# Kernel optimization log

Hardware: AMD Instinct MI355X
Metric: run time of the kernel (lower is better)

## Reference

```python
import jax, jax.numpy as jnp
import numpy as np

B, S, K = 8, 128, 12          # batch, seq len, nPredicts
DAR, DENC = 256, 256          # AR dim, encoder dim
NNEG = 128                    # negativeSamplingExt
W = S - K                     # windowSize


def setup_inputs() -> dict:
    key = jax.random.key(0)
    k1, k2, k3, k4, k5 = jax.random.split(key, 5)
    cFeature = jax.random.normal(k1, (B, S, DAR), dtype=jnp.float32)
    encodedData = jax.random.normal(k2, (B, S, DENC), dtype=jnp.float32)
    # stacked bias-free Linear weights, one per prediction step k
    Wpred = jax.random.normal(k3, (K, DENC, DAR), dtype=jnp.float32) / jnp.sqrt(DAR)
    n_idx = NNEG * W * B
    batchIdx = jax.random.randint(k4, (n_idx,), 0, B, dtype=jnp.int32)
    seqIdx = jax.random.randint(k5, (n_idx,), 1, S, dtype=jnp.int32)  # low=1 as in torch
    return {"cFeature": cFeature, "encodedData": encodedData, "Wpred": Wpred,
            "batchIdx": batchIdx, "seqIdx": seqIdx}


def reference(cFeature, encodedData, Wpred, batchIdx, seqIdx):
    c = cFeature[:, :W]                                   # (B, W, DAR)
    flat = encodedData.reshape(-1, DENC)                  # (B*S, DENC)

    # sampleClean: baseIdx arange(W) broadcast over (B, NNEG, W) then flattened
    base = jnp.tile(jnp.arange(W, dtype=jnp.int32), B * NNEG)
    seq = (seqIdx + base) % S
    ext = seq + batchIdx * S
    negExt = flat[ext].reshape(B, NNEG, W, DENC)          # irregular gather, ~121 MB

    # per-k linear prediction: locC[k] = c @ Wpred[k].T
    locC = jnp.einsum('bwd,ked->kbwe', c, Wpred)          # (K, B, W, DENC)

    # positives: encodedData[:, k:k+W] for k = 1..K
    pos = jnp.stack([encodedData[:, k:k + W] for k in range(1, K + 1)])  # (K, B, W, DENC)

    # (locC * candidates).mean(dim=feature) == dot / DENC
    posScore = jnp.einsum('kbwe,kbwe->kbw', locC, pos) / DENC           # (K, B, W)
    negScore = jnp.einsum('kbwe,bnwe->kbnw', locC, negExt) / DENC       # (K, B, N, W)

    logits = jnp.concatenate([posScore[:, :, None, :], negScore], axis=2)  # (K, B, 1+N, W)
    logits = jnp.transpose(logits, (0, 1, 3, 2)).reshape(K, B * W, 1 + NNEG)

    # cross entropy with label 0 (positive at class index 0)
    lse = jax.nn.logsumexp(logits, axis=-1)               # (K, B*W)
    losses = jnp.mean(lse - logits[..., 0], axis=-1)      # (K,)
    accs = jnp.mean((jnp.argmax(logits, axis=-1) == 0).astype(jnp.float32), axis=-1)
    return losses[None, :], accs[None, :]                  # (1, K), (1, K)
```

## Files before the change

kernel.cpp:

```cpp
#include <hip/hip_runtime.h>
#include <math.h>

#define B_    8
#define S_    128
#define K_    12
#define DAR_  256
#define DENC_ 256
#define NNEG_ 128
#define W_    116
#define BW_   928

typedef __attribute__((ext_vector_type(8))) short short8;
typedef __attribute__((ext_vector_type(4))) float floatx4;

static __device__ __forceinline__ unsigned short f2bf(float f) {
    union { float f; unsigned int u; } v; v.f = f;
    return (unsigned short)((v.u + 0x7FFFu + ((v.u >> 16) & 1u)) >> 16);
}

__global__ __launch_bounds__(256) void cast_all(
    const float* __restrict__ enc, const float* __restrict__ cf,
    const float* __restrict__ wp,
    unsigned short* __restrict__ ench, unsigned short* __restrict__ cfh,
    unsigned short* __restrict__ wph)
{
    const int g = blockIdx.x * 256 + threadIdx.x;
    const float* src; unsigned short* dst; int off;
    if (g < 32768)      { src = enc; dst = ench; off = g * 8; }
    else if (g < 65536) { src = cf;  dst = cfh;  off = (g - 32768) * 8; }
    else                { src = wp;  dst = wph;  off = (g - 65536) * 8; }
    float4 v0 = *(const float4*)(src + off);
    float4 v1 = *(const float4*)(src + off + 4);
    uint4 o;
    o.x = f2bf(v0.x) | ((unsigned)f2bf(v0.y) << 16);
    o.y = f2bf(v0.z) | ((unsigned)f2bf(v0.w) << 16);
    o.z = f2bf(v1.x) | ((unsigned)f2bf(v1.y) << 16);
    o.w = f2bf(v1.z) | ((unsigned)f2bf(v1.w) << 16);
    *(uint4*)(dst + off) = o;
}

__global__ __launch_bounds__(256) void stage1_mfma(
    const unsigned short* __restrict__ cfh,
    const unsigned short* __restrict__ wph,
    unsigned short* __restrict__ locCh)
{
    __shared__ unsigned short Bh[64 * 256];

    const int tid = threadIdx.x;
    const int mt = blockIdx.x;
    const int nt = blockIdx.y;
    const int k  = blockIdx.z;

    const int lane = tid & 63, wv = tid >> 6;
    const int l15 = lane & 15, quad = lane >> 4;

    const int am = mt * 64 + wv * 16 + l15;
    const bool avalid = (am < BW_);
    short8 a[8];
    if (avalid) {
        const int b = am / W_, w = am - b * W_;
        const unsigned short* arow = cfh + (size_t)(b * S_ + w) * 256;
#pragma unroll
        for (int kt = 0; kt < 8; ++kt)
            a[kt] = *(const short8*)(arow + kt * 32 + quad * 8);
    } else {
#pragma unroll
        for (int kt = 0; kt < 8; ++kt) a[kt] = short8{0,0,0,0,0,0,0,0};
    }

#pragma unroll
    for (int i = 0; i < 8; ++i) {
        const int flat = i * 256 + tid;
        const int row = flat >> 5, ch = flat & 31;
        const int e = nt * 64 + row;
        uint4 bv = *(const uint4*)(wph + ((size_t)(k * 256 + e) * 256 + ch * 8));
        *(uint4*)&Bh[(row * 32 + (ch ^ (row & 7))) * 8] = bv;
    }
    __syncthreads();

    floatx4 acc[4];
#pragma unroll
    for (int n4 = 0; n4 < 4; ++n4) {
        floatx4 c = {0.f, 0.f, 0.f, 0.f};
        const int bn = n4 * 16 + l15;
#pragma unroll
        for (int kt = 0; kt < 8; ++kt) {
            const int ch = kt * 4 + quad;
            short8 bfrag = *(const short8*)&Bh[(bn * 32 + (ch ^ (bn & 7))) * 8];
            c = __builtin_amdgcn_mfma_f32_16x16x32_bf16(a[kt], bfrag, c, 0, 0, 0);
        }
        acc[n4] = c;
    }

#pragma unroll
    for (int n4 = 0; n4 < 4; ++n4) {
        const int e = nt * 64 + n4 * 16 + l15;
#pragma unroll
        for (int r = 0; r < 4; ++r) {
            const int bwo = mt * 64 + wv * 16 + quad * 4 + r;
            if (bwo < BW_)
                locCh[((size_t)k * BW_ + bwo) * 256 + e] = f2bf(acc[r < 0 ? 0 : n4][r]);
        }
    }
}

__global__ __launch_bounds__(256) void stage2_mfma(
    const unsigned short* __restrict__ ench,
    const unsigned short* __restrict__ locCh,
    const int* __restrict__ batchIdx,
    const int* __restrict__ seqIdx,
    float* __restrict__ part)
{
    __shared__ int   idxL[144];
    __shared__ float sc[K_ * 132];

    const int tid = threadIdx.x;
    const int bw = blockIdx.x;
    const int b = bw / W_, w = bw - b * W_;

    const int lane = tid & 63, wv = tid >> 6;
    const int l15 = lane & 15, quad = lane >> 4;

    const int m = (l15 < K_) ? l15 : (K_ - 1);
    const unsigned short* arow = locCh + ((size_t)m * BW_ + bw) * 256;
    short8 a[8];
#pragma unroll
    for (int kt = 0; kt < 8; ++kt)
        a[kt] = *(const short8*)(arow + kt * 32 + quad * 8);

    if (tid < NNEG_) {
        const int ii = (b * NNEG_ + tid) * W_ + w;
        const int bi = batchIdx[ii];
        int si = seqIdx[ii] + w;
        if (si >= S_) si -= S_;
        idxL[tid] = bi * S_ + si;
    } else if (tid < 140) {
        idxL[tid] = b * S_ + w + 1 + (tid - 128);
    }
    __syncthreads();

    floatx4 accT[3];
#pragma unroll
    for (int u = 0; u < 3; ++u) {
        const int t = wv + u * 4;
        floatx4 c = {0.f, 0.f, 0.f, 0.f};
        if (t < 9) {
            const int n = t * 16 + l15;
            const int nn = (n < 140) ? n : 128;
            const unsigned short* brow = ench + (size_t)idxL[nn] * 256;
#pragma unroll
            for (int kt = 0; kt < 8; ++kt) {
                short8 bfrag = *(const short8*)(brow + kt * 32 + quad * 8);
                c = __builtin_amdgcn_mfma_f32_16x16x32_bf16(a[kt], bfrag, c, 0, 0, 0);
            }
        }
        accT[u] = c;
    }

    const float inv = 1.0f / 256.0f;
#pragma unroll
    for (int u = 0; u < 3; ++u) {
        const int t = wv + u * 4;
        if (t < 9) {
#pragma unroll
            for (int r = 0; r < 4; ++r) {
                const int mm = quad * 4 + r;
                if (mm < K_) {
                    const float val = accT[u][r] * inv;
                    if (t < 8)           sc[mm * 132 + t * 16 + l15] = val;
                    else if (l15 == mm)  sc[mm * 132 + 128] = val;
                }
            }
        }
    }
    __syncthreads();

    for (int k = wv; k < K_; k += 4) {
        const float x0  = sc[k * 132 + lane];
        const float x1  = sc[k * 132 + 64 + lane];
        const float pos = sc[k * 132 + 128];
        float mn = fmaxf(x0, x1);
#pragma unroll
        for (int o = 1; o < 64; o <<= 1) mn = fmaxf(mn, __shfl_xor(mn, o, 64));
        const float m2 = fmaxf(mn, pos);
        float s = __expf(x0 - m2) + __expf(x1 - m2);
#pragma unroll
        for (int o = 1; o < 64; o <<= 1) s += __shfl_xor(s, o, 64);
        if (lane == 0) {
            const float lse = m2 + __logf(s + __expf(pos - m2));
            part[k * BW_ + bw]        = lse - pos;
            part[(K_ + k) * BW_ + bw] = (pos >= mn) ? 1.0f : 0.0f;
        }
    }
}

__global__ __launch_bounds__(256) void stage3_reduce(
    const float* __restrict__ part, float* __restrict__ out)
{
    __shared__ float wsum[4];
    const int o = blockIdx.x, tid = threadIdx.x;
    float s = 0.f;
    for (int i = tid; i < BW_; i += 256) s += part[o * BW_ + i];
#pragma unroll
    for (int off = 1; off < 64; off <<= 1) s += __shfl_xor(s, off, 64);
    if ((tid & 63) == 0) wsum[tid >> 6] = s;
    __syncthreads();
    if (tid == 0)
        out[o] = (wsum[0] + wsum[1] + wsum[2] + wsum[3]) / (float)BW_;
}

extern "C" void kernel_launch(void* const* d_in, const int* in_sizes, int n_in,
                              void* d_out, int out_size, void* d_ws, size_t ws_size,
                              hipStream_t stream) {
    const float* cFeat    = (const float*)d_in[0];
    const float* enc      = (const float*)d_in[1];
    const float* Wp       = (const float*)d_in[2];
    const int*   batchIdx = (const int*)d_in[3];
    const int*   seqIdx   = (const int*)d_in[4];
    float* out = (float*)d_out;

    unsigned short* ench  = (unsigned short*)d_ws;
    unsigned short* cfh   = ench + 262144;
    unsigned short* wph   = cfh + 262144;
    unsigned short* locCh = wph + 786432;
    float*          part  = (float*)(locCh + (size_t)K_ * BW_ * 256);

    hipLaunchKernelGGL(cast_all, dim3(640), dim3(256), 0, stream,
                       enc, cFeat, Wp, ench, cfh, wph);
    hipLaunchKernelGGL(stage1_mfma, dim3(15, 4, 12), dim3(256), 0, stream,
                       cfh, wph, locCh);
    hipLaunchKernelGGL(stage2_mfma, dim3(BW_), dim3(256), 0, stream,
                       ench, locCh, batchIdx, seqIdx, part);
    hipLaunchKernelGGL(stage3_reduce, dim3(24), dim3(256), 0, stream,
                       part, out);
}
```

Before: 92.93 us.

## Fuse bf16 casts into stage1 and precompute transposed negative indices

Removes the separate cast kernel. Stage1 now reads fp32 cFeature and Wpred directly and converts them in registers. An extra column of stage1 blocks converts encodedData to bf16 and writes a precomputed, coalesced negative-index table indexed by (bw, n). Stage2 reads that table instead of doing strided gathers of batchIdx/seqIdx, and issues all its B-fragment loads before the MFMAs to expose memory parallelism. The trade-offs are more register pressure and doubled fp32 traffic in stage1 per tile reuse.

```diff
diff --git a/kernel.cpp b/kernel.cpp
--- a/kernel.cpp
+++ b/kernel.cpp
@@ -9,6 +9,7 @@
 #define NNEG_ 128
 #define W_    116
 #define BW_   928
+#define NIDX_ 118784
 
 typedef __attribute__((ext_vector_type(8))) short short8;
 typedef __attribute__((ext_vector_type(4))) float floatx4;
@@ -18,35 +19,48 @@
     return (unsigned short)((v.u + 0x7FFFu + ((v.u >> 16) & 1u)) >> 16);
 }
 
-__global__ __launch_bounds__(256) void cast_all(
-    const float* __restrict__ enc, const float* __restrict__ cf,
-    const float* __restrict__ wp,
-    unsigned short* __restrict__ ench, unsigned short* __restrict__ cfh,
-    unsigned short* __restrict__ wph)
-{
-    const int g = blockIdx.x * 256 + threadIdx.x;
-    const float* src; unsigned short* dst; int off;
-    if (g < 32768)      { src = enc; dst = ench; off = g * 8; }
-    else if (g < 65536) { src = cf;  dst = cfh;  off = (g - 32768) * 8; }
-    else                { src = wp;  dst = wph;  off = (g - 65536) * 8; }
-    float4 v0 = *(const float4*)(src + off);
-    float4 v1 = *(const float4*)(src + off + 4);
+static __device__ __forceinline__ uint4 pack2(float4 v0, float4 v1) {
     uint4 o;
     o.x = f2bf(v0.x) | ((unsigned)f2bf(v0.y) << 16);
     o.y = f2bf(v0.z) | ((unsigned)f2bf(v0.w) << 16);
     o.z = f2bf(v1.x) | ((unsigned)f2bf(v1.y) << 16);
     o.w = f2bf(v1.z) | ((unsigned)f2bf(v1.w) << 16);
-    *(uint4*)(dst + off) = o;
-}
-
-__global__ __launch_bounds__(256) void stage1_mfma(
-    const unsigned short* __restrict__ cfh,
-    const unsigned short* __restrict__ wph,
-    unsigned short* __restrict__ locCh)
+    return o;
+}
+
+__global__ __launch_bounds__(256, 2) void stage1_mfma(
+    const float* __restrict__ cFeat,
+    const float* __restrict__ Wp,
+    const float* __restrict__ enc,
+    const int* __restrict__ batchIdx,
+    const int* __restrict__ seqIdx,
+    unsigned short* __restrict__ ench,
+    unsigned short* __restrict__ locCh,
+    int* __restrict__ idxT)
 {
+    const int tid = threadIdx.x;
+
+    if (blockIdx.x == 15) {
+        const int ab = blockIdx.z * 4 + blockIdx.y;
+        for (int c = ab * 256 + tid; c < 32768; c += 48 * 256) {
+            float4 v0 = *(const float4*)(enc + c * 8);
+            float4 v1 = *(const float4*)(enc + c * 8 + 4);
+            *(uint4*)(ench + c * 8) = pack2(v0, v1);
+        }
+        for (int j = ab * 256 + tid; j < NIDX_; j += 48 * 256) {
+            const int n = j & 127, bw = j >> 7;
+            const int b = bw / W_, w = bw - b * W_;
+            const int ii = (b * NNEG_ + n) * W_ + w;
+            const int bi = batchIdx[ii];
+            int si = seqIdx[ii] + w;
+            if (si >= S_) si -= S_;
+            idxT[j] = bi * S_ + si;
+        }
+        return;
+    }
+
     __shared__ unsigned short Bh[64 * 256];
 
-    const int tid = threadIdx.x;
     const int mt = blockIdx.x;
     const int nt = blockIdx.y;
     const int k  = blockIdx.z;
@@ -55,26 +69,41 @@
     const int l15 = lane & 15, quad = lane >> 4;
 
     const int am = mt * 64 + wv * 16 + l15;
-    const bool avalid = (am < BW_);
-    short8 a[8];
-    if (avalid) {
-        const int b = am / W_, w = am - b * W_;
-        const unsigned short* arow = cfh + (size_t)(b * S_ + w) * 256;
-#pragma unroll
-        for (int kt = 0; kt < 8; ++kt)
-            a[kt] = *(const short8*)(arow + kt * 32 + quad * 8);
-    } else {
-#pragma unroll
-        for (int kt = 0; kt < 8; ++kt) a[kt] = short8{0,0,0,0,0,0,0,0};
-    }
-
+    float4 af[8][2];
+    const bool aval = (am < BW_);
+    {
+        const int bb = aval ? (am / W_) : 0;
+        const int ww = aval ? (am - bb * W_) : 0;
+        const float* arow = cFeat + (size_t)(bb * S_ + ww) * 256;
+#pragma unroll
+        for (int kt = 0; kt < 8; ++kt) {
+            af[kt][0] = *(const float4*)(arow + kt * 32 + quad * 8);
+            af[kt][1] = *(const float4*)(arow + kt * 32 + quad * 8 + 4);
+        }
+    }
+
+    float4 bf[8][2];
 #pragma unroll
     for (int i = 0; i < 8; ++i) {
         const int flat = i * 256 + tid;
         const int row = flat >> 5, ch = flat & 31;
-        const int e = nt * 64 + row;
-        uint4 bv = *(const uint4*)(wph + ((size_t)(k * 256 + e) * 256 + ch * 8));
-        *(uint4*)&Bh[(row * 32 + (ch ^ (row & 7))) * 8] = bv;
+        const float* p = Wp + ((size_t)(k * 256 + nt * 64 + row) * 256 + ch * 8);
+        bf[i][0] = *(const float4*)p;
+        bf[i][1] = *(const float4*)(p + 4);
+    }
+
+    short8 a[8];
+#pragma unroll
+    for (int kt = 0; kt < 8; ++kt) {
+        uint4 p = pack2(af[kt][0], af[kt][1]);
+        if (!aval) p = make_uint4(0, 0, 0, 0);
+        a[kt] = *(short8*)&p;
+    }
+#pragma unroll
+    for (int i = 0; i < 8; ++i) {
+        const int flat = i * 256 + tid;
+        const int row = flat >> 5, ch = flat & 31;
+        *(uint4*)&Bh[(row * 32 + (ch ^ (row & 7))) * 8] = pack2(bf[i][0], bf[i][1]);
     }
     __syncthreads();
 
@@ -99,16 +128,15 @@
         for (int r = 0; r < 4; ++r) {
             const int bwo = mt * 64 + wv * 16 + quad * 4 + r;
             if (bwo < BW_)
-                locCh[((size_t)k * BW_ + bwo) * 256 + e] = f2bf(acc[r < 0 ? 0 : n4][r]);
-        }
-    }
-}
-
-__global__ __launch_bounds__(256) void stage2_mfma(
+                locCh[((size_t)k * BW_ + bwo) * 256 + e] = f2bf(acc[n4][r]);
+        }
+    }
+}
+
+__global__ __launch_bounds__(256, 2) void stage2_mfma(
     const unsigned short* __restrict__ ench,
     const unsigned short* __restrict__ locCh,
-    const int* __restrict__ batchIdx,
-    const int* __restrict__ seqIdx,
+    const int* __restrict__ idxT,
     float* __restrict__ part)
 {
     __shared__ int   idxL[144];
@@ -128,32 +156,30 @@
     for (int kt = 0; kt < 8; ++kt)
         a[kt] = *(const short8*)(arow + kt * 32 + quad * 8);
 
-    if (tid < NNEG_) {
-        const int ii = (b * NNEG_ + tid) * W_ + w;
-        const int bi = batchIdx[ii];
-        int si = seqIdx[ii] + w;
-        if (si >= S_) si -= S_;
-        idxL[tid] = bi * S_ + si;
-    } else if (tid < 140) {
-        idxL[tid] = b * S_ + w + 1 + (tid - 128);
-    }
-    __syncthreads();
-
-    floatx4 accT[3];
+    if (tid < 128)      idxL[tid] = idxT[bw * 128 + tid];
+    else if (tid < 140) idxL[tid] = b * S_ + w + 1 + (tid - 128);
+    else if (tid < 144) idxL[tid] = b * S_ + w;
+    __syncthreads();
+
+    short8 bfr[3][8];
 #pragma unroll
     for (int u = 0; u < 3; ++u) {
         const int t = wv + u * 4;
+        const int n = t * 16 + l15;
+        const int nn = (t < 9) ? ((n < 140) ? n : 128) : 128;
+        const unsigned short* brow = ench + (size_t)idxL[nn] * 256;
+#pragma unroll
+        for (int kt = 0; kt < 8; ++kt)
+            bfr[u][kt] = *(const short8*)(brow + kt * 32 + quad * 8);
+    }
+
+    floatx4 accT[3];
+#pragma unroll
+    for (int u = 0; u < 3; ++u) {
         floatx4 c = {0.f, 0.f, 0.f, 0.f};
-        if (t < 9) {
-            const int n = t * 16 + l15;
-            const int nn = (n < 140) ? n : 128;
-            const unsigned short* brow = ench + (size_t)idxL[nn] * 256;
-#pragma unroll
-            for (int kt = 0; kt < 8; ++kt) {
-                short8 bfrag = *(const short8*)(brow + kt * 32 + quad * 8);
-                c = __builtin_amdgcn_mfma_f32_16x16x32_bf16(a[kt], bfrag, c, 0, 0, 0);
-            }
-        }
+#pragma unroll
+        for (int kt = 0; kt < 8; ++kt)
+            c = __builtin_amdgcn_mfma_f32_16x16x32_bf16(a[kt], bfr[u][kt], c, 0, 0, 0);
         accT[u] = c;
     }
 
@@ -220,17 +246,14 @@
     float* out = (float*)d_out;
 
     unsigned short* ench  = (unsigned short*)d_ws;
-    unsigned short* cfh   = ench + 262144;
-    unsigned short* wph   = cfh + 262144;
-    unsigned short* locCh = wph + 786432;
-    float*          part  = (float*)(locCh + (size_t)K_ * BW_ * 256);
-
-    hipLaunchKernelGGL(cast_all, dim3(640), dim3(256), 0, stream,
-                       enc, cFeat, Wp, ench, cfh, wph);
-    hipLaunchKernelGGL(stage1_mfma, dim3(15, 4, 12), dim3(256), 0, stream,
-                       cfh, wph, locCh);
+    unsigned short* locCh = ench + 262144;
+    int*   idxT = (int*)(locCh + (size_t)K_ * BW_ * 256);
+    float* part = (float*)(idxT + NIDX_);
+
+    hipLaunchKernelGGL(stage1_mfma, dim3(16, 4, 12), dim3(256), 0, stream,
+                       cFeat, Wp, enc, batchIdx, seqIdx, ench, locCh, idxT);
     hipLaunchKernelGGL(stage2_mfma, dim3(BW_), dim3(256), 0, stream,
-                       ench, locCh, batchIdx, seqIdx, part);
+                       ench, locCh, idxT, part);
     hipLaunchKernelGGL(stage3_reduce, dim3(24), dim3(256), 0, stream,
                        part, out);
 }
```

Result: slower. 95.85 us (+3.1%).
